# Performance work log

Measured on AMD Instinct MI355X. Metric: run time of the kernel, lower is better.

## Reference

```python
import jax, jax.numpy as jnp
import numpy as np
from jax import lax

DN = ('NCHW', 'OIHW', 'NCHW')
EPS = 1e-9
MASK_THR = 1e-3


def box_filter(x, size):
    # Separable box (ones) filter with SAME padding; x: [1,1,H,W]
    pad = size // 2
    kv = jnp.ones((1, 1, size, 1), x.dtype)
    kh = jnp.ones((1, 1, 1, size), x.dtype)
    y = lax.conv_general_dilated(x, kv, (1, 1), [(pad, pad), (0, 0)], dimension_numbers=DN)
    return lax.conv_general_dilated(y, kh, (1, 1), [(0, 0), (pad, pad)], dimension_numbers=DN)


def setup_inputs() -> dict:
    key = jax.random.key(0)
    k1, k2, k3, k4 = jax.random.split(key, 4)
    H = W = 2048
    I = jax.random.uniform(k1, (1, 1, H, W), jnp.float32)            # image in [0,1]
    u = jax.random.uniform(k2, (1, 4, H, W), jnp.float32)            # class memberships
    b = 1.0 + 0.1 * jax.random.normal(k3, (1, 1, H, W), jnp.float32)  # bias field ~1
    e = jax.random.normal(k4, (1, 1, H, W), jnp.float32) * 0.1       # residual
    return {"I": I, "u": u, "b": b, "e": e, "p": 2, "size": 21}


def reference(I, u, b, e, p, size):
    C = u.shape[1]
    e_d = lax.stop_gradient(e)
    b_d = lax.stop_gradient(b)
    up = u ** p                      # [1,C,H,W]
    b2 = b_d * b_d
    mask = (I > MASK_THR).astype(I.dtype)
    norm = box_filter(mask, size)    # partialFilter: local valid-pixel count

    def filt(x):                     # convParFilt: mask-normalized local mean
        return box_filter(x, size) / (norm + EPS)

    b_K = filt(b)
    b2_K = filt(b2)

    # classCenter (vectorized over classes 1..C-1)
    A = (I - e_d) * b_K                                   # [1,1,H,W]
    num = jnp.sum(A * up[:, 1:], axis=(0, 2, 3))          # [C-1]
    den = jnp.sum(b2_K * up[:, 1:], axis=(0, 2, 3))       # [C-1]
    c0 = jnp.sum(I * up[:, :1]) / (jnp.sum(up[:, :1]) + EPS)
    v = jnp.concatenate([c0[None], num / (den + EPS)])    # [C]

    # bias-field update: convolution is linear, so sum over classes first
    vb = v[None, :, None, None]
    bd = filt((I - e_d) * jnp.sum(vb * up, axis=1, keepdims=True))
    db = filt(jnp.sum(vb * vb * up, axis=1, keepdims=True))
    bd = bd * mask + (1.0 - mask)
    db = db * mask + (1.0 - mask)
    b_new = bd / (db + EPS)
    diff = b - b_new
    return jnp.mean(diff * diff)
```

## Files before the change

kernel.cpp:

```cpp
#include <hip/hip_runtime.h>

constexpr int Hh = 2048;
constexpr int Ww = 2048;
constexpr int NN = Hh * Ww;
constexpr int W4 = Ww / 4;
constexpr int NN4 = NN / 4;
constexpr int RAD = 10;
constexpr float EPSf = 1e-9f;
constexpr float MASK_THRf = 0.001f;
constexpr int CH = 8;
constexpr int BH = 16;
constexpr int NB = Hh / BH;
constexpr int TOTW = NB * Ww;
constexpr int NSLOT = 32;

__device__ inline float rcpf(float x) { return __builtin_amdgcn_rcpf(x); }

__device__ inline float waveReduce(float v) {
    #pragma unroll
    for (int o = 32; o > 0; o >>= 1) v += __shfl_down(v, o, 64);
    return v;
}

__device__ inline float4 f4zero() { float4 z; z.x = z.y = z.z = z.w = 0.f; return z; }
__device__ inline float4 f4add(float4 a, float4 b) {
    float4 r; r.x = a.x + b.x; r.y = a.y + b.y; r.z = a.z + b.z; r.w = a.w + b.w; return r;
}
__device__ inline float4 f4sub(float4 a, float4 b) {
    float4 r; r.x = a.x - b.x; r.y = a.y - b.y; r.z = a.z - b.z; r.w = a.w - b.w; return r;
}
__device__ inline void add4(float4& a, const float4 b) { a.x += b.x; a.y += b.y; a.z += b.z; a.w += b.w; }

__device__ inline void scan4(float v0, float v1, float v2, float v3, int lane,
                             float& carry, float P[4]) {
    float s0 = v0, s1 = s0 + v1, s2 = s1 + v2, s3 = s2 + v3;
    float T = s3;
    #pragma unroll
    for (int o = 1; o < 64; o <<= 1) {
        float t = __shfl_up(T, o, 64);
        if (lane >= o) T += t;
    }
    float base = T - s3 + carry;
    P[0] = base + s0; P[1] = base + s1; P[2] = base + s2; P[3] = base + s3;
    carry += __shfl(T, 63, 64);
}

__device__ inline float4 boxExtract(const float Pp[4], const float Pc[4], const float Pn[4], int lane) {
    int l2 = (lane + 2) & 63, l3 = (lane + 3) & 63;
    int m3 = (lane - 3) & 63, m2 = (lane - 2) & 63;
    bool c2 = (lane + 2) < 64, c3 = (lane + 3) < 64;
    bool g3 = lane >= 3, g2 = lane >= 2;
    float hc0 = __shfl(Pc[2], l2, 64), hn0 = __shfl(Pn[2], l2, 64);
    float hc1 = __shfl(Pc[3], l2, 64), hn1 = __shfl(Pn[3], l2, 64);
    float hc2 = __shfl(Pc[0], l3, 64), hn2 = __shfl(Pn[0], l3, 64);
    float hc3 = __shfl(Pc[1], l3, 64), hn3 = __shfl(Pn[1], l3, 64);
    float lc0 = __shfl(Pc[1], m3, 64), lp0 = __shfl(Pp[1], m3, 64);
    float lc1 = __shfl(Pc[2], m3, 64), lp1 = __shfl(Pp[2], m3, 64);
    float lc2 = __shfl(Pc[3], m3, 64), lp2 = __shfl(Pp[3], m3, 64);
    float lc3 = __shfl(Pc[0], m2, 64), lp3 = __shfl(Pp[0], m2, 64);
    float4 r;
    r.x = (c2 ? hc0 : hn0) - (g3 ? lc0 : lp0);
    r.y = (c2 ? hc1 : hn1) - (g3 ? lc1 : lp1);
    r.z = (c3 ? hc2 : hn2) - (g3 ? lc2 : lp2);
    r.w = (c3 ? hc3 : hn3) - (g2 ? lc3 : lp3);
    return r;
}

__global__ __launch_bounds__(256) void k1p(
        const float* __restrict__ I, const float* __restrict__ B,
        float* __restrict__ vpm, float* __restrict__ vpb, float* __restrict__ vpb2,
        float* __restrict__ tm, float* __restrict__ tb, float* __restrict__ tb2) {
    int x4 = blockIdx.x * 256 + threadIdx.x;
    int y0 = blockIdx.y * BH;
    const float4* I4 = (const float4*)I;
    const float4* B4 = (const float4*)B;
    float4 am = f4zero(), ab = f4zero(), ab2 = f4zero();
    #pragma unroll
    for (int r = 0; r < BH; ++r) {
        int idx = (y0 + r) * W4 + x4;
        float4 iv = I4[idx], bv = B4[idx];
        am.x += (iv.x > MASK_THRf) ? 1.f : 0.f;
        am.y += (iv.y > MASK_THRf) ? 1.f : 0.f;
        am.z += (iv.z > MASK_THRf) ? 1.f : 0.f;
        am.w += (iv.w > MASK_THRf) ? 1.f : 0.f;
        ab.x += bv.x; ab.y += bv.y; ab.z += bv.z; ab.w += bv.w;
        ab2.x += bv.x * bv.x; ab2.y += bv.y * bv.y;
        ab2.z += bv.z * bv.z; ab2.w += bv.w * bv.w;
        ((float4*)vpm)[idx] = am;
        ((float4*)vpb)[idx] = ab;
        ((float4*)vpb2)[idx] = ab2;
    }
    int t = blockIdx.y * W4 + x4;
    ((float4*)tm)[t] = am; ((float4*)tb)[t] = ab; ((float4*)tb2)[t] = ab2;
}

__global__ __launch_bounds__(256) void koff(
        const float* __restrict__ t0, const float* __restrict__ t1, const float* __restrict__ t2,
        float* __restrict__ o0, float* __restrict__ o1, float* __restrict__ o2) {
    int col = blockIdx.x * 256 + threadIdx.x;
    const float4* t; float4* o;
    if (blockIdx.y == 0)      { t = (const float4*)t0; o = (float4*)o0; }
    else if (blockIdx.y == 1) { t = (const float4*)t1; o = (float4*)o1; }
    else                      { t = (const float4*)t2; o = (float4*)o2; }
    float4 acc = f4zero();
    #pragma unroll 8
    for (int b = 0; b < NB; ++b) {
        o[b * W4 + col] = acc;
        float4 v = t[b * W4 + col];
        add4(acc, v);
    }
}

#define VBOX3(cc, vA, vB, vC, PA, PB, PC, OA, OB, OC) do { \
    int xo_ = (cc) * 64 + lane; \
    float4 uA_ = PA[upBase + xo_], uB_ = PB[upBase + xo_], uC_ = PC[upBase + xo_]; \
    float4 oA_ = OA[obUp + xo_], oB_ = OB[obUp + xo_], oC_ = OC[obUp + xo_]; \
    float4 dA_ = f4zero(), dB_ = f4zero(), dC_ = f4zero(); \
    float4 eA_ = f4zero(), eB_ = f4zero(), eC_ = f4zero(); \
    if (hasDn) { dA_ = PA[dnBase + xo_]; dB_ = PB[dnBase + xo_]; dC_ = PC[dnBase + xo_]; \
                 eA_ = OA[obDn + xo_]; eB_ = OB[obDn + xo_]; eC_ = OC[obDn + xo_]; } \
    vA = f4sub(f4add(uA_, oA_), f4add(dA_, eA_)); \
    vB = f4sub(f4add(uB_, oB_), f4add(dB_, eB_)); \
    vC = f4sub(f4add(uC_, oC_), f4add(dC_, eC_)); } while (0)

__device__ inline void k2_pix(float bm, float bb, float bb2, float Iv, float ev,
                              float u0, float u1, float u2, float u3, float* a) {
    float rn = rcpf(bm + EPSf);
    float bK = bb * rn;
    float b2K = bb2 * rn;
    float p0 = u0 * u0, p1 = u1 * u1, p2 = u2 * u2, p3 = u3 * u3;
    a[0] += Iv * p0;
    a[1] += p0;
    float A = (Iv - ev) * bK;
    a[2] += A * p1; a[3] += A * p2; a[4] += A * p3;
    a[5] += b2K * p1; a[6] += b2K * p2; a[7] += b2K * p3;
}

__global__ __launch_bounds__(256) void k2h(
        const float* __restrict__ vpm, const float* __restrict__ vpb, const float* __restrict__ vpb2,
        const float* __restrict__ om, const float* __restrict__ ob, const float* __restrict__ ob2,
        const float* __restrict__ I, const float* __restrict__ E, const float* __restrict__ U,
        float* __restrict__ accA) {
    int row = (blockIdx.x * 256 + threadIdx.x) >> 6;
    int lane = threadIdx.x & 63;
    int yup = row + RAD; if (yup > Hh - 1) yup = Hh - 1;
    int ydn = row - RAD - 1;
    bool hasDn = ydn >= 0;
    int upBase = yup * W4;
    int dnBase = hasDn ? ydn * W4 : 0;
    int obUp = (yup / BH) * W4;
    int obDn = hasDn ? (ydn / BH) * W4 : 0;
    int rowBase = row * W4;

    const float4* Pm = (const float4*)vpm;
    const float4* Pb = (const float4*)vpb;
    const float4* Pq = (const float4*)vpb2;
    const float4* Om = (const float4*)om;
    const float4* Ob = (const float4*)ob;
    const float4* Oq = (const float4*)ob2;
    const float4* I4 = (const float4*)I;
    const float4* E4 = (const float4*)E;
    const float4* U0 = (const float4*)U;
    const float4* U1 = U0 + NN4;
    const float4* U2 = U1 + NN4;
    const float4* U3 = U2 + NN4;

    float cm = 0.f, cb = 0.f, cq = 0.f;
    float Pm_p[4] = {0, 0, 0, 0}, Pb_p[4] = {0, 0, 0, 0}, Pq_p[4] = {0, 0, 0, 0};
    float Pm_c[4], Pb_c[4], Pq_c[4], Pm_n[4], Pb_n[4], Pq_n[4];
    float a[8] = {0, 0, 0, 0, 0, 0, 0, 0};

    {
        float4 vm, vb, vq;
        VBOX3(0, vm, vb, vq, Pm, Pb, Pq, Om, Ob, Oq);
        scan4(vm.x, vm.y, vm.z, vm.w, lane, cm, Pm_c);
        scan4(vb.x, vb.y, vb.z, vb.w, lane, cb, Pb_c);
        scan4(vq.x, vq.y, vq.z, vq.w, lane, cq, Pq_c);
    }
    #pragma unroll 1
    for (int c = 0; c < CH; ++c) {
        int xo = rowBase + c * 64 + lane;
        float4 Iv = I4[xo], Ev = E4[xo];
        float4 u0 = U0[xo], u1 = U1[xo], u2 = U2[xo], u3 = U3[xo];
        if (c + 1 < CH) {
            float4 vm, vb, vq;
            VBOX3(c + 1, vm, vb, vq, Pm, Pb, Pq, Om, Ob, Oq);
            scan4(vm.x, vm.y, vm.z, vm.w, lane, cm, Pm_n);
            scan4(vb.x, vb.y, vb.z, vb.w, lane, cb, Pb_n);
            scan4(vq.x, vq.y, vq.z, vq.w, lane, cq, Pq_n);
        } else {
            #pragma unroll
            for (int e = 0; e < 4; ++e) { Pm_n[e] = cm; Pb_n[e] = cb; Pq_n[e] = cq; }
        }
        float4 bm = boxExtract(Pm_p, Pm_c, Pm_n, lane);
        float4 bb = boxExtract(Pb_p, Pb_c, Pb_n, lane);
        float4 bq = boxExtract(Pq_p, Pq_c, Pq_n, lane);
        k2_pix(bm.x, bb.x, bq.x, Iv.x, Ev.x, u0.x, u1.x, u2.x, u3.x, a);
        k2_pix(bm.y, bb.y, bq.y, Iv.y, Ev.y, u0.y, u1.y, u2.y, u3.y, a);
        k2_pix(bm.z, bb.z, bq.z, Iv.z, Ev.z, u0.z, u1.z, u2.z, u3.z, a);
        k2_pix(bm.w, bb.w, bq.w, Iv.w, Ev.w, u0.w, u1.w, u2.w, u3.w, a);
        #pragma unroll
        for (int e = 0; e < 4; ++e) {
            Pm_p[e] = Pm_c[e]; Pb_p[e] = Pb_c[e]; Pq_p[e] = Pq_c[e];
            Pm_c[e] = Pm_n[e]; Pb_c[e] = Pb_n[e]; Pq_c[e] = Pq_n[e];
        }
    }

    __shared__ float sred[4][8];
    int wave = threadIdx.x >> 6;
    #pragma unroll
    for (int k = 0; k < 8; ++k) a[k] = waveReduce(a[k]);
    if (lane == 0) {
        #pragma unroll
        for (int k = 0; k < 8; ++k) sred[wave][k] = a[k];
    }
    __syncthreads();
    if (threadIdx.x < 8) {
        float s = sred[0][threadIdx.x] + sred[1][threadIdx.x] +
                  sred[2][threadIdx.x] + sred[3][threadIdx.x];
        atomicAdd(&accA[threadIdx.x * NSLOT + (blockIdx.x & (NSLOT - 1))], s);
    }
}

__global__ void k3_v(const float* __restrict__ accA, float* __restrict__ vV) {
    int lane = threadIdx.x;
    float s[8];
    #pragma unroll
    for (int k = 0; k < 8; ++k) {
        float v = (lane < NSLOT) ? accA[k * NSLOT + lane] : 0.f;
        s[k] = waveReduce(v);
    }
    if (lane == 0) {
        vV[0] = s[0] / (s[1] + EPSf);
        vV[1] = s[2] / (s[5] + EPSf);
        vV[2] = s[3] / (s[6] + EPSf);
        vV[3] = s[4] / (s[7] + EPSf);
    }
}

__global__ __launch_bounds__(256) void k4p(
        const float* __restrict__ I, const float* __restrict__ E, const float* __restrict__ U,
        const float* __restrict__ vV,
        float* __restrict__ vpP, float* __restrict__ vpQ,
        float* __restrict__ tP, float* __restrict__ tQ) {
    int x4 = blockIdx.x * 256 + threadIdx.x;
    int y0 = blockIdx.y * BH;
    float v0 = vV[0], v1 = vV[1], v2 = vV[2], v3 = vV[3];
    float w0 = v0 * v0, w1 = v1 * v1, w2 = v2 * v2, w3 = v3 * v3;
    const float4* I4 = (const float4*)I;
    const float4* E4 = (const float4*)E;
    const float4* U0 = (const float4*)U;
    const float4* U1 = U0 + NN4;
    const float4* U2 = U1 + NN4;
    const float4* U3 = U2 + NN4;
    float4 aP = f4zero(), aQ = f4zero();
    #pragma unroll
    for (int r = 0; r < BH; ++r) {
        int idx = (y0 + r) * W4 + x4;
        float4 Iv = I4[idx], Ev = E4[idx];
        float4 a0 = U0[idx], a1 = U1[idx], a2 = U2[idx], a3 = U3[idx];
        float p0, p1, p2, p3;
        p0 = a0.x * a0.x; p1 = a1.x * a1.x; p2 = a2.x * a2.x; p3 = a3.x * a3.x;
        aP.x += (Iv.x - Ev.x) * (v0 * p0 + v1 * p1 + v2 * p2 + v3 * p3);
        aQ.x += w0 * p0 + w1 * p1 + w2 * p2 + w3 * p3;
        p0 = a0.y * a0.y; p1 = a1.y * a1.y; p2 = a2.y * a2.y; p3 = a3.y * a3.y;
        aP.y += (Iv.y - Ev.y) * (v0 * p0 + v1 * p1 + v2 * p2 + v3 * p3);
        aQ.y += w0 * p0 + w1 * p1 + w2 * p2 + w3 * p3;
        p0 = a0.z * a0.z; p1 = a1.z * a1.z; p2 = a2.z * a2.z; p3 = a3.z * a3.z;
        aP.z += (Iv.z - Ev.z) * (v0 * p0 + v1 * p1 + v2 * p2 + v3 * p3);
        aQ.z += w0 * p0 + w1 * p1 + w2 * p2 + w3 * p3;
        p0 = a0.w * a0.w; p1 = a1.w * a1.w; p2 = a2.w * a2.w; p3 = a3.w * a3.w;
        aP.w += (Iv.w - Ev.w) * (v0 * p0 + v1 * p1 + v2 * p2 + v3 * p3);
        aQ.w += w0 * p0 + w1 * p1 + w2 * p2 + w3 * p3;
        ((float4*)vpP)[idx] = aP;
        ((float4*)vpQ)[idx] = aQ;
    }
    int t = blockIdx.y * W4 + x4;
    ((float4*)tP)[t] = aP; ((float4*)tQ)[t] = aQ;
}

__global__ __launch_bounds__(256) void k5h(
        const float* __restrict__ vpP, const float* __restrict__ vpQ, const float* __restrict__ vpm,
        const float* __restrict__ oP, const float* __restrict__ oQ, const float* __restrict__ om,
        const float* __restrict__ I, const float* __restrict__ B,
        float* __restrict__ accL) {
    int row = (blockIdx.x * 256 + threadIdx.x) >> 6;
    int lane = threadIdx.x & 63;
    int yup = row + RAD; if (yup > Hh - 1) yup = Hh - 1;
    int ydn = row - RAD - 1;
    bool hasDn = ydn >= 0;
    int upBase = yup * W4;
    int dnBase = hasDn ? ydn * W4 : 0;
    int obUp = (yup / BH) * W4;
    int obDn = hasDn ? (ydn / BH) * W4 : 0;
    int rowBase = row * W4;

    const float4* Pp4 = (const float4*)vpP;
    const float4* Pq4 = (const float4*)vpQ;
    const float4* Pm4 = (const float4*)vpm;
    const float4* Op4 = (const float4*)oP;
    const float4* Oq4 = (const float4*)oQ;
    const float4* Om4 = (const float4*)om;
    const float4* I4 = (const float4*)I;
    const float4* B4 = (const float4*)B;

    float cP = 0.f, cQ = 0.f, cm = 0.f;
    float PP_p[4] = {0, 0, 0, 0}, PQ_p[4] = {0, 0, 0, 0}, PM_p[4] = {0, 0, 0, 0};
    float PP_c[4], PQ_c[4], PM_c[4], PP_n[4], PQ_n[4], PM_n[4];
    float a = 0.f;

    {
        float4 vP, vQ, vm;
        VBOX3(0, vP, vQ, vm, Pp4, Pq4, Pm4, Op4, Oq4, Om4);
        scan4(vP.x, vP.y, vP.z, vP.w, lane, cP, PP_c);
        scan4(vQ.x, vQ.y, vQ.z, vQ.w, lane, cQ, PQ_c);
        scan4(vm.x, vm.y, vm.z, vm.w, lane, cm, PM_c);
    }
    #pragma unroll 1
    for (int c = 0; c < CH; ++c) {
        int xo = rowBase + c * 64 + lane;
        float4 Iv = I4[xo], Bv = B4[xo];
        if (c + 1 < CH) {
            float4 vP, vQ, vm;
            VBOX3(c + 1, vP, vQ, vm, Pp4, Pq4, Pm4, Op4, Oq4, Om4);
            scan4(vP.x, vP.y, vP.z, vP.w, lane, cP, PP_n);
            scan4(vQ.x, vQ.y, vQ.z, vQ.w, lane, cQ, PQ_n);
            scan4(vm.x, vm.y, vm.z, vm.w, lane, cm, PM_n);
        } else {
            #pragma unroll
            for (int e = 0; e < 4; ++e) { PP_n[e] = cP; PQ_n[e] = cQ; PM_n[e] = cm; }
        }
        float4 bP = boxExtract(PP_p, PP_c, PP_n, lane);
        float4 bQ = boxExtract(PQ_p, PQ_c, PQ_n, lane);
        float4 bM = boxExtract(PM_p, PM_c, PM_n, lane);
        {
            float rn = rcpf(bM.x + EPSf);
            float bd = bP.x * rn, db = bQ.x * rn;
            float m = (Iv.x > MASK_THRf) ? 1.f : 0.f;
            bd = bd * m + (1.f - m); db = db * m + (1.f - m);
            float d = Bv.x - bd * rcpf(db + EPSf); a += d * d;
        }
        {
            float rn = rcpf(bM.y + EPSf);
            float bd = bP.y * rn, db = bQ.y * rn;
            float m = (Iv.y > MASK_THRf) ? 1.f : 0.f;
            bd = bd * m + (1.f - m); db = db * m + (1.f - m);
            float d = Bv.y - bd * rcpf(db + EPSf); a += d * d;
        }
        {
            float rn = rcpf(bM.z + EPSf);
            float bd = bP.z * rn, db = bQ.z * rn;
            float m = (Iv.z > MASK_THRf) ? 1.f : 0.f;
            bd = bd * m + (1.f - m); db = db * m + (1.f - m);
            float d = Bv.z - bd * rcpf(db + EPSf); a += d * d;
        }
        {
            float rn = rcpf(bM.w + EPSf);
            float bd = bP.w * rn, db = bQ.w * rn;
            float m = (Iv.w > MASK_THRf) ? 1.f : 0.f;
            bd = bd * m + (1.f - m); db = db * m + (1.f - m);
            float d = Bv.w - bd * rcpf(db + EPSf); a += d * d;
        }
        #pragma unroll
        for (int e = 0; e < 4; ++e) {
            PP_p[e] = PP_c[e]; PQ_p[e] = PQ_c[e]; PM_p[e] = PM_c[e];
            PP_c[e] = PP_n[e]; PQ_c[e] = PQ_n[e]; PM_c[e] = PM_n[e];
        }
    }

    a = waveReduce(a);
    __shared__ float sred[4];
    int wave = threadIdx.x >> 6;
    if (lane == 0) sred[wave] = a;
    __syncthreads();
    if (threadIdx.x == 0) {
        atomicAdd(&accL[blockIdx.x & (NSLOT - 1)], sred[0] + sred[1] + sred[2] + sred[3]);
    }
}

__global__ void k6_out(const float* __restrict__ accL, float* __restrict__ out) {
    int lane = threadIdx.x;
    float v = (lane < NSLOT) ? accL[lane] : 0.f;
    v = waveReduce(v);
    if (lane == 0) out[0] = v / (float)NN;
}

extern "C" void kernel_launch(void* const* d_in, const int* in_sizes, int n_in,
                              void* d_out, int out_size, void* d_ws, size_t ws_size,
                              hipStream_t stream) {
    const float* I = (const float*)d_in[0];
    const float* U = (const float*)d_in[1];
    const float* B = (const float*)d_in[2];
    const float* E = (const float*)d_in[3];

    float* vpm  = (float*)d_ws;
    float* vpb  = vpm + NN;
    float* vpb2 = vpb + NN;
    float* tm   = vpb2 + NN;
    float* tb   = tm + TOTW;
    float* tb2  = tb + TOTW;
    float* om   = tb2 + TOTW;
    float* ob   = om + TOTW;
    float* ob2  = ob + TOTW;
    float* accA = ob2 + TOTW;
    float* accL = accA + 8 * NSLOT;
    float* vV   = accL + NSLOT;

    hipMemsetAsync(accA, 0, (8 * NSLOT + NSLOT) * sizeof(float), stream);

    dim3 blk(256);
    dim3 gband(2, NB);
    int hblocks = Hh / 4;

    k1p<<<gband, blk, 0, stream>>>(I, B, vpm, vpb, vpb2, tm, tb, tb2);
    koff<<<dim3(2, 3), blk, 0, stream>>>(tm, tb, tb2, om, ob, ob2);
    k2h<<<hblocks, blk, 0, stream>>>(vpm, vpb, vpb2, om, ob, ob2, I, E, U, accA);
    k3_v<<<1, 64, 0, stream>>>(accA, vV);
    k4p<<<gband, blk, 0, stream>>>(I, E, U, vV, vpb, vpb2, tm, tb);
    koff<<<dim3(2, 2), blk, 0, stream>>>(tm, tb, tb2, ob, ob2, om);
    k5h<<<hblocks, blk, 0, stream>>>(vpb, vpb2, vpm, ob, ob2, om, I, B, accL);
    k6_out<<<1, 64, 0, stream>>>(accL, (float*)d_out);
}
```

Baseline: 235.4 us.

## Split horizontal box pass into overlapping wave segments with shuffle window sum

The horizontal box pass in k2 and k5 used to give each wave a full row, walking eight chunks sequentially with a wave prefix scan and carry. Now each wave handles a 58-float4 segment plus a 3-lane halo on each side, and computes the 21-wide window directly from neighbour shuffles. This removes the serial per-row scan chain and raises the number of waves, exposing more parallelism and memory-level concurrency. The cost is redundant halo loads of the vertical-sum inputs (64 lanes loaded for 58 useful) and idle halo lanes during the per-pixel compute.

Result: slower. 276.3 us (+17.3%).

```diff
diff --git a/kernel.cpp b/kernel.cpp
--- a/kernel.cpp
+++ b/kernel.cpp
@@ -8,11 +8,13 @@
 constexpr int RAD = 10;
 constexpr float EPSf = 1e-9f;
 constexpr float MASK_THRf = 0.001f;
-constexpr int CH = 8;
 constexpr int BH = 16;
 constexpr int NB = Hh / BH;
 constexpr int TOTW = NB * Ww;
 constexpr int NSLOT = 32;
+constexpr int SEGW = 58;
+constexpr int NSEG = 9;
+constexpr int HBLOCKS = Hh * NSEG / 4;
 
 __device__ inline float rcpf(float x) { return __builtin_amdgcn_rcpf(x); }
 
@@ -31,38 +33,24 @@
 }
 __device__ inline void add4(float4& a, const float4 b) { a.x += b.x; a.y += b.y; a.z += b.z; a.w += b.w; }
 
-__device__ inline void scan4(float v0, float v1, float v2, float v3, int lane,
-                             float& carry, float P[4]) {
-    float s0 = v0, s1 = s0 + v1, s2 = s1 + v2, s3 = s2 + v3;
-    float T = s3;
-    #pragma unroll
-    for (int o = 1; o < 64; o <<= 1) {
-        float t = __shfl_up(T, o, 64);
-        if (lane >= o) T += t;
-    }
-    float base = T - s3 + carry;
-    P[0] = base + s0; P[1] = base + s1; P[2] = base + s2; P[3] = base + s3;
-    carry += __shfl(T, 63, 64);
-}
-
-__device__ inline float4 boxExtract(const float Pp[4], const float Pc[4], const float Pn[4], int lane) {
-    int l2 = (lane + 2) & 63, l3 = (lane + 3) & 63;
-    int m3 = (lane - 3) & 63, m2 = (lane - 2) & 63;
-    bool c2 = (lane + 2) < 64, c3 = (lane + 3) < 64;
-    bool g3 = lane >= 3, g2 = lane >= 2;
-    float hc0 = __shfl(Pc[2], l2, 64), hn0 = __shfl(Pn[2], l2, 64);
-    float hc1 = __shfl(Pc[3], l2, 64), hn1 = __shfl(Pn[3], l2, 64);
-    float hc2 = __shfl(Pc[0], l3, 64), hn2 = __shfl(Pn[0], l3, 64);
-    float hc3 = __shfl(Pc[1], l3, 64), hn3 = __shfl(Pn[1], l3, 64);
-    float lc0 = __shfl(Pc[1], m3, 64), lp0 = __shfl(Pp[1], m3, 64);
-    float lc1 = __shfl(Pc[2], m3, 64), lp1 = __shfl(Pp[2], m3, 64);
-    float lc2 = __shfl(Pc[3], m3, 64), lp2 = __shfl(Pp[3], m3, 64);
-    float lc3 = __shfl(Pc[0], m2, 64), lp3 = __shfl(Pp[0], m2, 64);
+__device__ inline float4 hbox(float4 v, int lane) {
+    float S = v.x + v.y + v.z + v.w;
+    float Sm2 = __shfl(S, lane - 2, 64);
+    float Sm1 = __shfl(S, lane - 1, 64);
+    float Sp1 = __shfl(S, lane + 1, 64);
+    float Sp2 = __shfl(S, lane + 2, 64);
+    float T5 = Sm2 + Sm1 + S + Sp1 + Sp2;
+    float wm3 = __shfl(v.w, lane - 3, 64);
+    float zm3 = __shfl(v.z, lane - 3, 64);
+    float xm2 = __shfl(v.x, lane - 2, 64);
+    float wp2 = __shfl(v.w, lane + 2, 64);
+    float xp3 = __shfl(v.x, lane + 3, 64);
+    float yp3 = __shfl(v.y, lane + 3, 64);
     float4 r;
-    r.x = (c2 ? hc0 : hn0) - (g3 ? lc0 : lp0);
-    r.y = (c2 ? hc1 : hn1) - (g3 ? lc1 : lp1);
-    r.z = (c3 ? hc2 : hn2) - (g3 ? lc2 : lp2);
-    r.w = (c3 ? hc3 : hn3) - (g2 ? lc3 : lp3);
+    r.y = T5 + wm3;
+    r.z = T5 + xp3;
+    r.x = r.y + zm3 - wp2;
+    r.w = r.z + yp3 - xm2;
     return r;
 }
 
@@ -111,18 +99,6 @@
     }
 }
 
-#define VBOX3(cc, vA, vB, vC, PA, PB, PC, OA, OB, OC) do { \
-    int xo_ = (cc) * 64 + lane; \
-    float4 uA_ = PA[upBase + xo_], uB_ = PB[upBase + xo_], uC_ = PC[upBase + xo_]; \
-    float4 oA_ = OA[obUp + xo_], oB_ = OB[obUp + xo_], oC_ = OC[obUp + xo_]; \
-    float4 dA_ = f4zero(), dB_ = f4zero(), dC_ = f4zero(); \
-    float4 eA_ = f4zero(), eB_ = f4zero(), eC_ = f4zero(); \
-    if (hasDn) { dA_ = PA[dnBase + xo_]; dB_ = PB[dnBase + xo_]; dC_ = PC[dnBase + xo_]; \
-                 eA_ = OA[obDn + xo_]; eB_ = OB[obDn + xo_]; eC_ = OC[obDn + xo_]; } \
-    vA = f4sub(f4add(uA_, oA_), f4add(dA_, eA_)); \
-    vB = f4sub(f4add(uB_, oB_), f4add(dB_, eB_)); \
-    vC = f4sub(f4add(uC_, oC_), f4add(dC_, eC_)); } while (0)
-
 __device__ inline void k2_pix(float bm, float bb, float bb2, float Iv, float ev,
                               float u0, float u1, float u2, float u3, float* a) {
     float rn = rcpf(bm + EPSf);
@@ -136,21 +112,26 @@
     a[5] += b2K * p1; a[6] += b2K * p2; a[7] += b2K * p3;
 }
 
-__global__ __launch_bounds__(256) void k2h(
+__global__ __launch_bounds__(256) void k2s(
         const float* __restrict__ vpm, const float* __restrict__ vpb, const float* __restrict__ vpb2,
         const float* __restrict__ om, const float* __restrict__ ob, const float* __restrict__ ob2,
         const float* __restrict__ I, const float* __restrict__ E, const float* __restrict__ U,
         float* __restrict__ accA) {
-    int row = (blockIdx.x * 256 + threadIdx.x) >> 6;
     int lane = threadIdx.x & 63;
+    int wid = blockIdx.x * 4 + (threadIdx.x >> 6);
+    int row = wid / NSEG;
+    int seg = wid - row * NSEG;
+    int xc = seg * SEGW - 3 + lane;
+    bool inb = (unsigned)xc < (unsigned)W4;
+    int xl = inb ? xc : 0;
+
     int yup = row + RAD; if (yup > Hh - 1) yup = Hh - 1;
     int ydn = row - RAD - 1;
     bool hasDn = ydn >= 0;
-    int upBase = yup * W4;
-    int dnBase = hasDn ? ydn * W4 : 0;
-    int obUp = (yup / BH) * W4;
-    int obDn = hasDn ? (ydn / BH) * W4 : 0;
-    int rowBase = row * W4;
+    int upBase = yup * W4 + xl;
+    int dnBase = (hasDn ? ydn * W4 : 0) + xl;
+    int obUp = (yup / BH) * W4 + xl;
+    int obDn = (hasDn ? (ydn / BH) * W4 : 0) + xl;
 
     const float4* Pm = (const float4*)vpm;
     const float4* Pb = (const float4*)vpb;
@@ -158,52 +139,38 @@
     const float4* Om = (const float4*)om;
     const float4* Ob = (const float4*)ob;
     const float4* Oq = (const float4*)ob2;
-    const float4* I4 = (const float4*)I;
-    const float4* E4 = (const float4*)E;
-    const float4* U0 = (const float4*)U;
-    const float4* U1 = U0 + NN4;
-    const float4* U2 = U1 + NN4;
-    const float4* U3 = U2 + NN4;
-
-    float cm = 0.f, cb = 0.f, cq = 0.f;
-    float Pm_p[4] = {0, 0, 0, 0}, Pb_p[4] = {0, 0, 0, 0}, Pq_p[4] = {0, 0, 0, 0};
-    float Pm_c[4], Pb_c[4], Pq_c[4], Pm_n[4], Pb_n[4], Pq_n[4];
+
+    float4 vm = f4zero(), vb = f4zero(), vq = f4zero();
+    if (inb) {
+        vm = f4add(Pm[upBase], Om[obUp]);
+        vb = f4add(Pb[upBase], Ob[obUp]);
+        vq = f4add(Pq[upBase], Oq[obUp]);
+        if (hasDn) {
+            vm = f4sub(vm, f4add(Pm[dnBase], Om[obDn]));
+            vb = f4sub(vb, f4add(Pb[dnBase], Ob[obDn]));
+            vq = f4sub(vq, f4add(Pq[dnBase], Oq[obDn]));
+        }
+    }
+
+    float4 bm = hbox(vm, lane);
+    float4 bb = hbox(vb, lane);
+    float4 bq = hbox(vq, lane);
+
     float a[8] = {0, 0, 0, 0, 0, 0, 0, 0};
-
-    {
-        float4 vm, vb, vq;
-        VBOX3(0, vm, vb, vq, Pm, Pb, Pq, Om, Ob, Oq);
-        scan4(vm.x, vm.y, vm.z, vm.w, lane, cm, Pm_c);
-        scan4(vb.x, vb.y, vb.z, vb.w, lane, cb, Pb_c);
-        scan4(vq.x, vq.y, vq.z, vq.w, lane, cq, Pq_c);
-    }
-    #pragma unroll 1
-    for (int c = 0; c < CH; ++c) {
-        int xo = rowBase + c * 64 + lane;
+    if (inb && lane >= 3 && lane <= 60) {
+        const float4* I4 = (const float4*)I;
+        const float4* E4 = (const float4*)E;
+        const float4* U0 = (const float4*)U;
+        const float4* U1 = U0 + NN4;
+        const float4* U2 = U1 + NN4;
+        const float4* U3 = U2 + NN4;
+        int xo = row * W4 + xc;
         float4 Iv = I4[xo], Ev = E4[xo];
         float4 u0 = U0[xo], u1 = U1[xo], u2 = U2[xo], u3 = U3[xo];
-        if (c + 1 < CH) {
-            float4 vm, vb, vq;
-            VBOX3(c + 1, vm, vb, vq, Pm, Pb, Pq, Om, Ob, Oq);
-            scan4(vm.x, vm.y, vm.z, vm.w, lane, cm, Pm_n);
-            scan4(vb.x, vb.y, vb.z, vb.w, lane, cb, Pb_n);
-            scan4(vq.x, vq.y, vq.z, vq.w, lane, cq, Pq_n);
-        } else {
-            #pragma unroll
-            for (int e = 0; e < 4; ++e) { Pm_n[e] = cm; Pb_n[e] = cb; Pq_n[e] = cq; }
-        }
-        float4 bm = boxExtract(Pm_p, Pm_c, Pm_n, lane);
-        float4 bb = boxExtract(Pb_p, Pb_c, Pb_n, lane);
-        float4 bq = boxExtract(Pq_p, Pq_c, Pq_n, lane);
         k2_pix(bm.x, bb.x, bq.x, Iv.x, Ev.x, u0.x, u1.x, u2.x, u3.x, a);
         k2_pix(bm.y, bb.y, bq.y, Iv.y, Ev.y, u0.y, u1.y, u2.y, u3.y, a);
         k2_pix(bm.z, bb.z, bq.z, Iv.z, Ev.z, u0.z, u1.z, u2.z, u3.z, a);
         k2_pix(bm.w, bb.w, bq.w, Iv.w, Ev.w, u0.w, u1.w, u2.w, u3.w, a);
-        #pragma unroll
-        for (int e = 0; e < 4; ++e) {
-            Pm_p[e] = Pm_c[e]; Pb_p[e] = Pb_c[e]; Pq_p[e] = Pq_c[e];
-            Pm_c[e] = Pm_n[e]; Pb_c[e] = Pb_n[e]; Pq_c[e] = Pq_n[e];
-        }
     }
 
     __shared__ float sred[4][8];
@@ -279,21 +246,26 @@
     ((float4*)tP)[t] = aP; ((float4*)tQ)[t] = aQ;
 }
 
-__global__ __launch_bounds__(256) void k5h(
+__global__ __launch_bounds__(256) void k5s(
         const float* __restrict__ vpP, const float* __restrict__ vpQ, const float* __restrict__ vpm,
         const float* __restrict__ oP, const float* __restrict__ oQ, const float* __restrict__ om,
         const float* __restrict__ I, const float* __restrict__ B,
         float* __restrict__ accL) {
-    int row = (blockIdx.x * 256 + threadIdx.x) >> 6;
     int lane = threadIdx.x & 63;
+    int wid = blockIdx.x * 4 + (threadIdx.x >> 6);
+    int row = wid / NSEG;
+    int seg = wid - row * NSEG;
+    int xc = seg * SEGW - 3 + lane;
+    bool inb = (unsigned)xc < (unsigned)W4;
+    int xl = inb ? xc : 0;
+
     int yup = row + RAD; if (yup > Hh - 1) yup = Hh - 1;
     int ydn = row - RAD - 1;
     bool hasDn = ydn >= 0;
-    int upBase = yup * W4;
-    int dnBase = hasDn ? ydn * W4 : 0;
-    int obUp = (yup / BH) * W4;
-    int obDn = hasDn ? (ydn / BH) * W4 : 0;
-    int rowBase = row * W4;
+    int upBase = yup * W4 + xl;
+    int dnBase = (hasDn ? ydn * W4 : 0) + xl;
+    int obUp = (yup / BH) * W4 + xl;
+    int obDn = (hasDn ? (ydn / BH) * W4 : 0) + xl;
 
     const float4* Pp4 = (const float4*)vpP;
     const float4* Pq4 = (const float4*)vpQ;
@@ -301,38 +273,29 @@
     const float4* Op4 = (const float4*)oP;
     const float4* Oq4 = (const float4*)oQ;
     const float4* Om4 = (const float4*)om;
-    const float4* I4 = (const float4*)I;
-    const float4* B4 = (const float4*)B;
-
-    float cP = 0.f, cQ = 0.f, cm = 0.f;
-    float PP_p[4] = {0, 0, 0, 0}, PQ_p[4] = {0, 0, 0, 0}, PM_p[4] = {0, 0, 0, 0};
-    float PP_c[4], PQ_c[4], PM_c[4], PP_n[4], PQ_n[4], PM_n[4];
+
+    float4 vP = f4zero(), vQ = f4zero(), vM = f4zero();
+    if (inb) {
+        vP = f4add(Pp4[upBase], Op4[obUp]);
+        vQ = f4add(Pq4[upBase], Oq4[obUp]);
+        vM = f4add(Pm4[upBase], Om4[obUp]);
+        if (hasDn) {
+            vP = f4sub(vP, f4add(Pp4[dnBase], Op4[obDn]));
+            vQ = f4sub(vQ, f4add(Pq4[dnBase], Oq4[obDn]));
+            vM = f4sub(vM, f4add(Pm4[dnBase], Om4[obDn]));
+        }
+    }
+
+    float4 bP = hbox(vP, lane);
+    float4 bQ = hbox(vQ, lane);
+    float4 bM = hbox(vM, lane);
+
     float a = 0.f;
-
-    {
-        float4 vP, vQ, vm;
-        VBOX3(0, vP, vQ, vm, Pp4, Pq4, Pm4, Op4, Oq4, Om4);
-        scan4(vP.x, vP.y, vP.z, vP.w, lane, cP, PP_c);
-        scan4(vQ.x, vQ.y, vQ.z, vQ.w, lane, cQ, PQ_c);
-        scan4(vm.x, vm.y, vm.z, vm.w, lane, cm, PM_c);
-    }
-    #pragma unroll 1
-    for (int c = 0; c < CH; ++c) {
-        int xo = rowBase + c * 64 + lane;
+    if (inb && lane >= 3 && lane <= 60) {
+        const float4* I4 = (const float4*)I;
+        const float4* B4 = (const float4*)B;
+        int xo = row * W4 + xc;
         float4 Iv = I4[xo], Bv = B4[xo];
-        if (c + 1 < CH) {
-            float4 vP, vQ, vm;
-            VBOX3(c + 1, vP, vQ, vm, Pp4, Pq4, Pm4, Op4, Oq4, Om4);
-            scan4(vP.x, vP.y, vP.z, vP.w, lane, cP, PP_n);
-            scan4(vQ.x, vQ.y, vQ.z, vQ.w, lane, cQ, PQ_n);
-            scan4(vm.x, vm.y, vm.z, vm.w, lane, cm, PM_n);
-        } else {
-            #pragma unroll
-            for (int e = 0; e < 4; ++e) { PP_n[e] = cP; PQ_n[e] = cQ; PM_n[e] = cm; }
-        }
-        float4 bP = boxExtract(PP_p, PP_c, PP_n, lane);
-        float4 bQ = boxExtract(PQ_p, PQ_c, PQ_n, lane);
-        float4 bM = boxExtract(PM_p, PM_c, PM_n, lane);
         {
             float rn = rcpf(bM.x + EPSf);
             float bd = bP.x * rn, db = bQ.x * rn;
@@ -360,11 +323,6 @@
             float m = (Iv.w > MASK_THRf) ? 1.f : 0.f;
             bd = bd * m + (1.f - m); db = db * m + (1.f - m);
             float d = Bv.w - bd * rcpf(db + EPSf); a += d * d;
-        }
-        #pragma unroll
-        for (int e = 0; e < 4; ++e) {
-            PP_p[e] = PP_c[e]; PQ_p[e] = PQ_c[e]; PM_p[e] = PM_c[e];
-            PP_c[e] = PP_n[e]; PQ_c[e] = PQ_n[e]; PM_c[e] = PM_n[e];
         }
     }
 
@@ -410,14 +368,13 @@
 
     dim3 blk(256);
     dim3 gband(2, NB);
-    int hblocks = Hh / 4;
 
     k1p<<<gband, blk, 0, stream>>>(I, B, vpm, vpb, vpb2, tm, tb, tb2);
     koff<<<dim3(2, 3), blk, 0, stream>>>(tm, tb, tb2, om, ob, ob2);
-    k2h<<<hblocks, blk, 0, stream>>>(vpm, vpb, vpb2, om, ob, ob2, I, E, U, accA);
+    k2s<<<HBLOCKS, blk, 0, stream>>>(vpm, vpb, vpb2, om, ob, ob2, I, E, U, accA);
     k3_v<<<1, 64, 0, stream>>>(accA, vV);
     k4p<<<gband, blk, 0, stream>>>(I, E, U, vV, vpb, vpb2, tm, tb);
     koff<<<dim3(2, 2), blk, 0, stream>>>(tm, tb, tb2, ob, ob2, om);
-    k5h<<<hblocks, blk, 0, stream>>>(vpb, vpb2, vpm, ob, ob2, om, I, B, accL);
+    k5s<<<HBLOCKS, blk, 0, stream>>>(vpb, vpb2, vpm, ob, ob2, om, I, B, accL);
     k6_out<<<1, 64, 0, stream>>>(accL, (float*)d_out);
 }
```
